# Performance work log

Hardware: AMD Instinct MI355X
Metric: run time of the kernel (lower is better)

The kernel has to match this reference:

```python
import jax, jax.numpy as jnp
import numpy as np

N = 30000      # num_nodes
E = 480000     # num_edges
NF = 128       # node_features
EF = 64        # edge_features
HID = 256      # hidden_dim
L = 4          # num_layers
H = 8          # heads
D = HID // H   # per-head dim = 32
SCALE = 0.02


def _ln(x, g, b, eps=1e-5):
    m = x.mean(-1, keepdims=True)
    v = ((x - m) ** 2).mean(-1, keepdims=True)
    return (x - m) * jax.lax.rsqrt(v + eps) * g + b


def _mlp_head(x, W1, b1, W2, b2):
    return jax.nn.sigmoid(jax.nn.relu(x @ W1 + b1) @ W2 + b2)


def setup_inputs() -> dict:
    key = jax.random.key(0)
    ks = jax.random.split(key, 32)
    r = lambda k, shp: SCALE * jax.random.normal(k, shp, dtype=jnp.float32)
    inp = {
        'x': jax.random.normal(ks[0], (N, NF), dtype=jnp.float32),
        'edge_attr': jax.random.normal(ks[1], (E, EF), dtype=jnp.float32),
        'edge_index': jax.random.randint(ks[2], (2, E), 0, N, dtype=jnp.int32),
        # encoders
        'enc_Wn': r(ks[3], (NF, HID)), 'enc_bn': jnp.zeros((HID,), jnp.float32),
        'enc_We': r(ks[4], (EF, HID)), 'enc_be': jnp.zeros((HID,), jnp.float32),
        # stacked TransformerConv params for L layers
        'Wq': r(ks[5], (L, HID, HID)), 'bq': jnp.zeros((L, HID), jnp.float32),
        'Wk': r(ks[6], (L, HID, HID)), 'bk': jnp.zeros((L, HID), jnp.float32),
        'Wv': r(ks[7], (L, HID, HID)), 'bv': jnp.zeros((L, HID), jnp.float32),
        'We': r(ks[8], (L, HID, HID)),  # lin_edge has no bias in PyG
        'Wsk': r(ks[9], (L, HID, HID)), 'bsk': jnp.zeros((L, HID), jnp.float32),
        # shared LayerNorm (module reuses self.norm every layer)
        'ln_g': jnp.ones((HID,), jnp.float32), 'ln_b': jnp.zeros((HID,), jnp.float32),
        # contagion predictor
        'cp_W1': r(ks[10], (HID, HID // 2)), 'cp_b1': jnp.zeros((HID // 2,), jnp.float32),
        'cp_W2': r(ks[11], (HID // 2, 1)), 'cp_b2': jnp.zeros((1,), jnp.float32),
        # systemic risk predictor
        'sp_W1': r(ks[12], (HID, HID // 2)), 'sp_b1': jnp.zeros((HID // 2,), jnp.float32),
        'sp_W2': r(ks[13], (HID // 2, 1)), 'sp_b2': jnp.zeros((1,), jnp.float32),
    }
    return inp


def reference(x, edge_attr, edge_index, enc_Wn, enc_bn, enc_We, enc_be,
              Wq, bq, Wk, bk, Wv, bv, We, Wsk, bsk, ln_g, ln_b,
              cp_W1, cp_b1, cp_W2, cp_b2, sp_W1, sp_b1, sp_W2, sp_b2):
    src, dst = edge_index[0], edge_index[1]
    h = x @ enc_Wn + enc_bn                 # [N,HID]
    e = edge_attr @ enc_We + enc_be         # [E,HID]
    inv_sqrt_d = 1.0 / jnp.sqrt(jnp.asarray(D, h.dtype))
    for l in range(L):
        # TransformerConv: query at dst, key/value at src, edge bias on both k and v
        q = (h @ Wq[l] + bq[l]).reshape(N, H, D)[dst]            # [E,H,D]
        ke = (e @ We[l]).reshape(E, H, D)                        # [E,H,D]
        k = (h @ Wk[l] + bk[l]).reshape(N, H, D)[src] + ke
        v = (h @ Wv[l] + bv[l]).reshape(N, H, D)[src] + ke
        score = (q * k).sum(-1) * inv_sqrt_d                     # [E,H]
        smax = jax.ops.segment_max(score, dst, num_segments=N)   # [N,H]
        p = jnp.exp(score - smax[dst])
        denom = jax.ops.segment_sum(p, dst, num_segments=N)
        alpha = p / (denom[dst] + 1e-16)                         # scatter-softmax
        agg = jax.ops.segment_sum(alpha[..., None] * v, dst, num_segments=N)
        out = agg.reshape(N, HID) + h @ Wsk[l] + bsk[l]          # concat heads + root skip
        h = _ln(h + out, ln_g, ln_b)                             # residual + shared LN (eval: no dropout)
    g = h.mean(0, keepdims=True)                                 # [1,HID] global mean pool
    contagion_risk = _mlp_head(h, cp_W1, cp_b1, cp_W2, cp_b2)    # [N,1]
    systemic_risk = _mlp_head(g, sp_W1, sp_b1, sp_W2, sp_b2)     # [1,1]
    return h, g, contagion_risk, systemic_risk
```

## Files before the change

kernel.cpp:

```cpp
#include <hip/hip_runtime.h>
#include <cstddef>
#include <cstdint>

#define NN 30000
#define EE 480000
#define NFD 128
#define EFD 64
#define HID 256
#define NL 4
#define NH 8

#define DT_BF16 0
#define DT_F32  1
#define DT_EXT  2

#define OFF_WT  ((size_t)65787648)
#define MIN_B   ((size_t)68015872)
#define MIN_A   ((size_t)129455872)

#define WT_ENC 0
#define WT_LAYER(l) (32768 + (size_t)(l) * 262144)
#define WT_CP1 (32768 + (size_t)1048576)

typedef short bf16x8 __attribute__((ext_vector_type(8)));
typedef unsigned short us8 __attribute__((ext_vector_type(8)));
typedef float f32x4 __attribute__((ext_vector_type(4)));

__device__ __forceinline__ float bf2f(unsigned short u) {
  union { unsigned int i; float f; } v; v.i = ((unsigned int)u) << 16; return v.f;
}
__device__ __forceinline__ unsigned short f2bf(float f) {
  union { float f; unsigned int i; } v; v.f = f;
  unsigned int i = v.i;
  return (unsigned short)((i + 0x7FFFu + ((i >> 16) & 1u)) >> 16);
}
struct F4 { float x, y, z, w; };
__device__ __forceinline__ F4 load4bf(const unsigned short* p) {
  ushort4 u = *reinterpret_cast<const ushort4*>(p);
  F4 f; f.x = bf2f(u.x); f.y = bf2f(u.y); f.z = bf2f(u.z); f.w = bf2f(u.w);
  return f;
}
__device__ __forceinline__ F4 load4f(const float* p) {
  float4 t = *reinterpret_cast<const float4*>(p);
  F4 f; f.x = t.x; f.y = t.y; f.z = t.z; f.w = t.w; return f;
}
__device__ __forceinline__ F4 load4any(const void* p, size_t idx, int f32) {
  return f32 ? load4f((const float*)p + idx) : load4bf((const unsigned short*)p + idx);
}
__device__ __forceinline__ float load1any(const void* p, size_t idx, int f32) {
  return f32 ? ((const float*)p)[idx] : bf2f(((const unsigned short*)p)[idx]);
}
__device__ __forceinline__ void store1any(void* p, size_t idx, float v, int f32) {
  if (f32) ((float*)p)[idx] = v; else ((unsigned short*)p)[idx] = f2bf(v);
}

__global__ void probe_dtype(const void* __restrict__ ln_g, int* __restrict__ flag) {
  unsigned int u = *(const unsigned int*)ln_g;
  *flag = ((u & 0xFFFFu) == 0u) ? 1 : 0;
}

__global__ void wt_build(const void* __restrict__ enc_Wn,
                         const void* __restrict__ Wq, const void* __restrict__ Wk,
                         const void* __restrict__ Wv, const void* __restrict__ Wsk,
                         const void* __restrict__ cp_W1,
                         unsigned short* __restrict__ Wt, const int* __restrict__ flagp)
{
  const int f = *flagp;
  size_t idx = (size_t)blockIdx.x * 256 + threadIdx.x;
  if (idx < 32768) {
    int n = idx >> 7, k = idx & 127;
    Wt[WT_ENC + idx] = f2bf(load1any(enc_Wn, (size_t)k * 256 + n, f));
  } else if (idx < 32768 + 1048576) {
    size_t off = idx - 32768;
    int l = off >> 18;
    int which = (off >> 16) & 3;
    size_t e = off & 65535;
    int n = e >> 8, k = e & 255;
    const void* W = (which == 0) ? Wq : (which == 1) ? Wk : (which == 2) ? Wv : Wsk;
    Wt[idx] = f2bf(load1any(W, (size_t)l * 65536 + (size_t)k * 256 + n, f));
  } else if (idx < 32768 + 1048576 + 32768) {
    size_t e = idx - 32768 - 1048576;
    int n = e >> 8, k = e & 255;
    Wt[idx] = f2bf(load1any(cp_W1, (size_t)k * 128 + n, f));
  }
}

template<bool OUT_F32, bool RELU>
__global__ __launch_bounds__(256) void mfma_gemm(
    const void* __restrict__ Av, int aMode,
    const unsigned short* __restrict__ Bt,
    const void* __restrict__ biasv, size_t biasEl, int biasMode,
    void* __restrict__ Cv, int ldC, int cOff,
    int M, int K, const int* __restrict__ flagp)
{
  const int f = *flagp;
  const int aF32 = (aMode == DT_EXT) ? f : aMode;
  const int biF32 = (biasMode == DT_EXT) ? f : biasMode;

  __shared__ unsigned short Al[128][40];
  __shared__ unsigned short Bl[64][40];
  const int bm = blockIdx.x * 128;
  const int bn = blockIdx.y * 64;
  const int tid = threadIdx.x;
  const int wv = tid >> 6, lane = tid & 63;
  const int l16 = lane & 15, quad = lane >> 4;

  f32x4 acc[2][4];
#pragma unroll
  for (int i = 0; i < 2; i++)
#pragma unroll
    for (int j = 0; j < 4; j++) acc[i][j] = (f32x4){0.f, 0.f, 0.f, 0.f};

  const int ar = tid >> 1;
  const int ah = (tid & 1) << 4;
  const int bnr = tid >> 2;
  const int bk8 = (tid & 3) << 3;

  for (int k0 = 0; k0 < K; k0 += 32) {
    us8 w0, w1;
    int gr = bm + ar;
    if (gr < M) {
      if (!aF32) {
        const unsigned short* ap = (const unsigned short*)Av + (size_t)gr * K + k0 + ah;
        w0 = *(const us8*)ap;
        w1 = *(const us8*)(ap + 8);
      } else {
        const float* ap = (const float*)Av + (size_t)gr * K + k0 + ah;
        float4 u0 = *(const float4*)ap;
        float4 u1 = *(const float4*)(ap + 4);
        float4 u2 = *(const float4*)(ap + 8);
        float4 u3 = *(const float4*)(ap + 12);
        w0[0] = f2bf(u0.x); w0[1] = f2bf(u0.y); w0[2] = f2bf(u0.z); w0[3] = f2bf(u0.w);
        w0[4] = f2bf(u1.x); w0[5] = f2bf(u1.y); w0[6] = f2bf(u1.z); w0[7] = f2bf(u1.w);
        w1[0] = f2bf(u2.x); w1[1] = f2bf(u2.y); w1[2] = f2bf(u2.z); w1[3] = f2bf(u2.w);
        w1[4] = f2bf(u3.x); w1[5] = f2bf(u3.y); w1[6] = f2bf(u3.z); w1[7] = f2bf(u3.w);
      }
    } else {
      w0 = (us8)0; w1 = (us8)0;
    }
    *(us8*)&Al[ar][ah] = w0;
    *(us8*)&Al[ar][ah + 8] = w1;
    *(us8*)&Bl[bnr][bk8] = *(const us8*)&Bt[(size_t)(bn + bnr) * K + k0 + bk8];
    __syncthreads();

    bf16x8 a0 = *(const bf16x8*)&Al[wv * 32 + l16][quad * 8];
    bf16x8 a1 = *(const bf16x8*)&Al[wv * 32 + 16 + l16][quad * 8];
#pragma unroll
    for (int tn = 0; tn < 4; tn++) {
      bf16x8 b = *(const bf16x8*)&Bl[tn * 16 + l16][quad * 8];
      acc[0][tn] = __builtin_amdgcn_mfma_f32_16x16x32_bf16(a0, b, acc[0][tn], 0, 0, 0);
      acc[1][tn] = __builtin_amdgcn_mfma_f32_16x16x32_bf16(a1, b, acc[1][tn], 0, 0, 0);
    }
    __syncthreads();
  }

#pragma unroll
  for (int tm = 0; tm < 2; tm++) {
#pragma unroll
    for (int tn = 0; tn < 4; tn++) {
      int col = bn + tn * 16 + l16;
      float bias = load1any(biasv, biasEl + col, biF32);
#pragma unroll
      for (int r = 0; r < 4; r++) {
        int row = bm + wv * 32 + tm * 16 + quad * 4 + r;
        if (row < M) {
          float v = acc[tm][tn][r] + bias;
          if (RELU) v = fmaxf(v, 0.f);
          size_t off = (size_t)row * ldC + cOff + col;
          if (OUT_F32) ((float*)Cv)[off] = v;
          else ((unsigned short*)Cv)[off] = f2bf(v);
        }
      }
    }
  }
}

__global__ __launch_bounds__(256) void mfma_gemm_qkvs(
    const unsigned short* __restrict__ A,
    const unsigned short* __restrict__ Bt,
    const void* __restrict__ bq, const void* __restrict__ bk,
    const void* __restrict__ bv, const void* __restrict__ bsk, size_t biasEl,
    unsigned short* __restrict__ Qb, unsigned short* __restrict__ KVb,
    unsigned short* __restrict__ Sb,
    int M, const int* __restrict__ flagp)
{
  const int f = *flagp;
  __shared__ unsigned short Al[128][40];
  __shared__ unsigned short Bl[64][40];
  const int bm = blockIdx.x * 128;
  const int bnG = blockIdx.y * 64;
  const int which = bnG >> 8;
  const int bn = bnG & 255;
  const int tid = threadIdx.x;
  const int wv = tid >> 6, lane = tid & 63;
  const int l16 = lane & 15, quad = lane >> 4;

  f32x4 acc[2][4];
#pragma unroll
  for (int i = 0; i < 2; i++)
#pragma unroll
    for (int j = 0; j < 4; j++) acc[i][j] = (f32x4){0.f, 0.f, 0.f, 0.f};

  const int ar = tid >> 1;
  const int ah = (tid & 1) << 4;
  const int bnr = tid >> 2;
  const int bk8 = (tid & 3) << 3;
  const unsigned short* Bbase = Bt + (size_t)which * 65536;

  for (int k0 = 0; k0 < HID; k0 += 32) {
    us8 w0, w1;
    int gr = bm + ar;
    if (gr < M) {
      const unsigned short* ap = A + (size_t)gr * HID + k0 + ah;
      w0 = *(const us8*)ap;
      w1 = *(const us8*)(ap + 8);
    } else {
      w0 = (us8)0; w1 = (us8)0;
    }
    *(us8*)&Al[ar][ah] = w0;
    *(us8*)&Al[ar][ah + 8] = w1;
    *(us8*)&Bl[bnr][bk8] = *(const us8*)&Bbase[(size_t)(bn + bnr) * HID + k0 + bk8];
    __syncthreads();

    bf16x8 a0 = *(const bf16x8*)&Al[wv * 32 + l16][quad * 8];
    bf16x8 a1 = *(const bf16x8*)&Al[wv * 32 + 16 + l16][quad * 8];
#pragma unroll
    for (int tn = 0; tn < 4; tn++) {
      bf16x8 b = *(const bf16x8*)&Bl[tn * 16 + l16][quad * 8];
      acc[0][tn] = __builtin_amdgcn_mfma_f32_16x16x32_bf16(a0, b, acc[0][tn], 0, 0, 0);
      acc[1][tn] = __builtin_amdgcn_mfma_f32_16x16x32_bf16(a1, b, acc[1][tn], 0, 0, 0);
    }
    __syncthreads();
  }

  const void* biasv = (which == 0) ? bq : (which == 1) ? bk : (which == 2) ? bv : bsk;
  unsigned short* out = (which == 0) ? Qb : (which == 3) ? Sb : KVb;
  const int ldC = (which == 1 || which == 2) ? 512 : 256;
  const int cOff = (which == 2) ? 256 : 0;

#pragma unroll
  for (int tm = 0; tm < 2; tm++) {
#pragma unroll
    for (int tn = 0; tn < 4; tn++) {
      int col = bn + tn * 16 + l16;
      float bias = load1any(biasv, biasEl + col, f);
#pragma unroll
      for (int r = 0; r < 4; r++) {
        int row = bm + wv * 32 + tm * 16 + quad * 4 + r;
        if (row < M)
          out[(size_t)row * ldC + cOff + col] = f2bf(acc[tm][tn][r] + bias);
      }
    }
  }
}

__global__ void fold_kernel(const void* __restrict__ enc_We,
                            const void* __restrict__ enc_be,
                            const void* __restrict__ We_all,
                            float* __restrict__ Mfold, const int* __restrict__ flagp)
{
  const int f = *flagp;
  int idx = blockIdx.x * blockDim.x + threadIdx.x;
  if (idx >= NL * 65 * HID) return;
  int l = idx / (65 * HID);
  int rc = idx - l * 65 * HID;
  int row = rc >> 8;
  int col = rc & 255;
  size_t Wbase = (size_t)l * HID * HID;
  float acc = 0.f;
  if (row < 64) {
    for (int k = 0; k < HID; k++)
      acc += load1any(enc_We, (size_t)row * HID + k, f) * load1any(We_all, Wbase + (size_t)k * HID + col, f);
  } else {
    for (int k = 0; k < HID; k++)
      acc += load1any(enc_be, k, f) * load1any(We_all, Wbase + (size_t)k * HID + col, f);
  }
  Mfold[idx] = acc;
}

__global__ void hist_kernel(const int* __restrict__ dst, int* __restrict__ rp) {
  int e = blockIdx.x * 256 + threadIdx.x;
  if (e < EE) atomicAdd(&rp[dst[e]], 1);
}

__global__ __launch_bounds__(1024) void scan_kernel(int* __restrict__ rp) {
  __shared__ int part[1024];
  int t = threadIdx.x;
  int base = t * 30;
  int loc[30];
  int sum = 0;
#pragma unroll
  for (int i = 0; i < 30; i++) {
    int idx = base + i;
    int v = (idx < NN) ? rp[idx] : 0;
    loc[i] = v; sum += v;
  }
  part[t] = sum;
  __syncthreads();
  for (int off = 1; off < 1024; off <<= 1) {
    int v = (t >= off) ? part[t - off] : 0;
    __syncthreads();
    part[t] += v;
    __syncthreads();
  }
  int run = (t == 0) ? 0 : part[t - 1];
#pragma unroll
  for (int i = 0; i < 30; i++) {
    int idx = base + i;
    if (idx < NN) { rp[idx] = run; run += loc[i]; }
    else if (idx == NN) { rp[NN] = run; }
  }
}

__global__ void scatter_kernel(const int* __restrict__ src, const int* __restrict__ dst,
                               const int* __restrict__ rp, int* __restrict__ cnt2,
                               int2* __restrict__ sed) {
  int e = blockIdx.x * 256 + threadIdx.x;
  if (e >= EE) return;
  int d = dst[e];
  int pos = rp[d] + atomicAdd(&cnt2[d], 1);
  int2 v; v.x = src[e]; v.y = e;
  sed[pos] = v;
}

__global__ void ea_build(const int2* __restrict__ sed, const void* __restrict__ edge_attr,
                         unsigned short* __restrict__ ea_srt, const int* __restrict__ flagp) {
  const int f = *flagp;
  int gid = blockIdx.x * 256 + threadIdx.x;
  int pos = gid >> 4;
  int sub = (gid & 15) * 4;
  int e = sed[pos].y;
  F4 v = load4any(edge_attr, (size_t)e * EFD + sub, f);
  ushort4 o; o.x = f2bf(v.x); o.y = f2bf(v.y); o.z = f2bf(v.z); o.w = f2bf(v.w);
  *reinterpret_cast<ushort4*>(ea_srt + (size_t)pos * EFD + sub) = o;
}

template<bool SORTED>
__global__ __launch_bounds__(256, 6) void edge_fused(
    const int* __restrict__ rp, const int2* __restrict__ sed,
    const unsigned short* __restrict__ Qb, const unsigned short* __restrict__ KV,
    const unsigned short* __restrict__ ea_srt,
    const void* __restrict__ edge_attr,
    const float* __restrict__ Mf,
    const unsigned short* __restrict__ Sb,
    unsigned short* __restrict__ hb,
    const void* __restrict__ ln_g, const void* __restrict__ ln_b,
    const int* __restrict__ flagp)
{
  __shared__ float wl[4][8][68];
  const int f = *flagp;
  const int wv = __builtin_amdgcn_readfirstlane(threadIdx.x >> 6);
  const int nw = blockIdx.x * 4 + wv;
  const int lane = threadIdx.x & 63;
  const int hd = lane >> 3;
  const int j = lane & 7;
  const int jb = j << 3;
  const int c4 = lane * 4;

  const size_t rowb = (size_t)nw * HID;
  F4 q4 = load4bf(Qb + rowb + c4);

  float t8[8] = {0.f, 0.f, 0.f, 0.f, 0.f, 0.f, 0.f, 0.f};
#pragma unroll
  for (int cc = 0; cc < 8; cc++) {
    F4 qc = load4bf(Qb + rowb + hd * 32 + cc * 4);
#pragma unroll
    for (int kk = 0; kk < 8; kk++) {
      const float4 m4 = *reinterpret_cast<const float4*>(
          Mf + (size_t)(jb + kk) * HID + hd * 32 + cc * 4);
      float a = t8[kk];
      a = fmaf(m4.x, qc.x, a);
      a = fmaf(m4.y, qc.y, a);
      a = fmaf(m4.z, qc.z, a);
      a = fmaf(m4.w, qc.w, a);
      t8[kk] = a;
    }
  }
  float s0;
  {
    F4 b4 = load4f(Mf + (size_t)64 * HID + c4);
    s0 = q4.x * b4.x + q4.y * b4.y + q4.z * b4.z + q4.w * b4.w;
    s0 += __shfl_xor(s0, 1);
    s0 += __shfl_xor(s0, 2);
    s0 += __shfl_xor(s0, 4);
  }

  float accv[4] = {0.f, 0.f, 0.f, 0.f};
  float wacc[8] = {0.f, 0.f, 0.f, 0.f, 0.f, 0.f, 0.f, 0.f};
  float den = 0.f;
  const int beg = rp[nw], end = rp[nw + 1];

  if (beg < end) {
    const float scl = 0.17677669529663687f;
    int tA = beg;
    int tB = (beg + 1 < end) ? beg + 1 : beg;
    int sA = sed[tA].x;
    int sB = sed[tB].x;
    const unsigned short* kvp;
    kvp = KV + (size_t)sA * 512;
    F4 kA = load4bf(kvp + c4);
    F4 vA = load4bf(kvp + 256 + c4);
    kvp = KV + (size_t)sB * 512;
    F4 kB = load4bf(kvp + c4);
    F4 vB = load4bf(kvp + 256 + c4);
    F4 ea0A, ea1A, ea0B, ea1B;
    if (SORTED) {
      ea0A = load4bf(ea_srt + (size_t)tA * EFD + j * 8);
      ea1A = load4bf(ea_srt + (size_t)tA * EFD + j * 8 + 4);
      ea0B = load4bf(ea_srt + (size_t)tB * EFD + j * 8);
      ea1B = load4bf(ea_srt + (size_t)tB * EFD + j * 8 + 4);
    } else {
      size_t eA = (size_t)sed[tA].y, eB = (size_t)sed[tB].y;
      ea0A = load4any(edge_attr, eA * EFD + j * 8, f);
      ea1A = load4any(edge_attr, eA * EFD + j * 8 + 4, f);
      ea0B = load4any(edge_attr, eB * EFD + j * 8, f);
      ea1B = load4any(edge_attr, eB * EFD + j * 8 + 4, f);
    }
    int tC = (beg + 2 < end) ? beg + 2 : beg;
    int tD = (beg + 3 < end) ? beg + 3 : beg;
    int sC = sed[tC].x;
    int sD = sed[tD].x;

    for (int t = beg; t < end; t += 2) {
      kvp = KV + (size_t)sC * 512;
      F4 kC = load4bf(kvp + c4);
      F4 vC = load4bf(kvp + 256 + c4);
      kvp = KV + (size_t)sD * 512;
      F4 kD = load4bf(kvp + c4);
      F4 vD = load4bf(kvp + 256 + c4);
      F4 ea0C, ea1C, ea0D, ea1D;
      if (SORTED) {
        ea0C = load4bf(ea_srt + (size_t)tC * EFD + j * 8);
        ea1C = load4bf(ea_srt + (size_t)tC * EFD + j * 8 + 4);
        ea0D = load4bf(ea_srt + (size_t)tD * EFD + j * 8);
        ea1D = load4bf(ea_srt + (size_t)tD * EFD + j * 8 + 4);
      } else {
        size_t eC = (size_t)sed[tC].y, eD = (size_t)sed[tD].y;
        ea0C = load4any(edge_attr, eC * EFD + j * 8, f);
        ea1C = load4any(edge_attr, eC * EFD + j * 8 + 4, f);
        ea0D = load4any(edge_attr, eD * EFD + j * 8, f);
        ea1D = load4any(edge_attr, eD * EFD + j * 8 + 4, f);
      }
      int tE = (t + 4 < end) ? t + 4 : beg;
      int tF = (t + 5 < end) ? t + 5 : beg;
      int sE = sed[tE].x;
      int sF = sed[tF].x;

      float mB = (t + 1 < end) ? 1.f : 0.f;
      float rA = q4.x * kA.x + q4.y * kA.y + q4.z * kA.z + q4.w * kA.w;
      float rB = q4.x * kB.x + q4.y * kB.y + q4.z * kB.z + q4.w * kB.w;
      rA = fmaf(ea0A.x, t8[0], rA); rB = fmaf(ea0B.x, t8[0], rB);
      rA = fmaf(ea0A.y, t8[1], rA); rB = fmaf(ea0B.y, t8[1], rB);
      rA = fmaf(ea0A.z, t8[2], rA); rB = fmaf(ea0B.z, t8[2], rB);
      rA = fmaf(ea0A.w, t8[3], rA); rB = fmaf(ea0B.w, t8[3], rB);
      rA = fmaf(ea1A.x, t8[4], rA); rB = fmaf(ea1B.x, t8[4], rB);
      rA = fmaf(ea1A.y, t8[5], rA); rB = fmaf(ea1B.y, t8[5], rB);
      rA = fmaf(ea1A.z, t8[6], rA); rB = fmaf(ea1B.z, t8[6], rB);
      rA = fmaf(ea1A.w, t8[7], rA); rB = fmaf(ea1B.w, t8[7], rB);
      { float u = __shfl_xor(rA, 1); float v = __shfl_xor(rB, 1); rA += u; rB += v; }
      { float u = __shfl_xor(rA, 2); float v = __shfl_xor(rB, 2); rA += u; rB += v; }
      { float u = __shfl_xor(rA, 4); float v = __shfl_xor(rB, 4); rA += u; rB += v; }
      float scA = fminf(fmaxf((rA + s0) * scl, -30.f), 30.f);
      float scB = fminf(fmaxf((rB + s0) * scl, -30.f), 30.f);
      float pA = __expf(scA);
      float pB = mB * __expf(scB);
      den += pA + pB;
      accv[0] = fmaf(pA, vA.x, fmaf(pB, vB.x, accv[0]));
      accv[1] = fmaf(pA, vA.y, fmaf(pB, vB.y, accv[1]));
      accv[2] = fmaf(pA, vA.z, fmaf(pB, vB.z, accv[2]));
      accv[3] = fmaf(pA, vA.w, fmaf(pB, vB.w, accv[3]));
      wacc[0] = fmaf(pA, ea0A.x, fmaf(pB, ea0B.x, wacc[0]));
      wacc[1] = fmaf(pA, ea0A.y, fmaf(pB, ea0B.y, wacc[1]));
      wacc[2] = fmaf(pA, ea0A.z, fmaf(pB, ea0B.z, wacc[2]));
      wacc[3] = fmaf(pA, ea0A.w, fmaf(pB, ea0B.w, wacc[3]));
      wacc[4] = fmaf(pA, ea1A.x, fmaf(pB, ea1B.x, wacc[4]));
      wacc[5] = fmaf(pA, ea1A.y, fmaf(pB, ea1B.y, wacc[5]));
      wacc[6] = fmaf(pA, ea1A.z, fmaf(pB, ea1B.z, wacc[6]));
      wacc[7] = fmaf(pA, ea1A.w, fmaf(pB, ea1B.w, wacc[7]));
      kA = kC; vA = vC; ea0A = ea0C; ea1A = ea1C;
      kB = kD; vB = vD; ea0B = ea0D; ea1B = ea1D;
      tA = tC; tB = tD; tC = tE; tD = tF; sC = sE; sD = sF;
    }
  }

#pragma unroll
  for (int i = 0; i < 8; i++) wl[wv][hd][jb + i] = wacc[i];
  __syncthreads();

  float ke0 = 0.f, ke1 = 0.f, ke2 = 0.f, ke3 = 0.f;
#pragma unroll 8
  for (int k = 0; k < 64; k++) {
    float w = wl[wv][hd][k];
    float4 m4 = *reinterpret_cast<const float4*>(Mf + (size_t)k * HID + c4);
    ke0 = fmaf(w, m4.x, ke0);
    ke1 = fmaf(w, m4.y, ke1);
    ke2 = fmaf(w, m4.z, ke2);
    ke3 = fmaf(w, m4.w, ke3);
  }

  float invden = 1.f / (den + 1e-16f);
  float sel = (end > beg) ? 1.f : 0.f;
  F4 b4 = load4f(Mf + (size_t)64 * HID + c4);
  F4 s4 = load4bf(Sb + rowb + c4);
  F4 hh = load4bf(hb + rowb + c4);
  float r0 = hh.x + sel * ((accv[0] + ke0) * invden + b4.x) + s4.x;
  float r1 = hh.y + sel * ((accv[1] + ke1) * invden + b4.y) + s4.y;
  float r2 = hh.z + sel * ((accv[2] + ke2) * invden + b4.z) + s4.z;
  float r3 = hh.w + sel * ((accv[3] + ke3) * invden + b4.w) + s4.w;

  float sum = r0 + r1 + r2 + r3;
#pragma unroll
  for (int o = 1; o < 64; o <<= 1) sum += __shfl_xor(sum, o);
  float mean = sum * (1.f / HID);
  float d0 = r0 - mean, d1 = r1 - mean, d2 = r2 - mean, d3 = r3 - mean;
  float vs = d0 * d0 + d1 * d1 + d2 * d2 + d3 * d3;
#pragma unroll
  for (int o = 1; o < 64; o <<= 1) vs += __shfl_xor(vs, o);
  float rstd = rsqrtf(vs * (1.f / HID) + 1e-5f);
  ushort4 o4;
  o4.x = f2bf(d0 * rstd * load1any(ln_g, c4 + 0, f) + load1any(ln_b, c4 + 0, f));
  o4.y = f2bf(d1 * rstd * load1any(ln_g, c4 + 1, f) + load1any(ln_b, c4 + 1, f));
  o4.z = f2bf(d2 * rstd * load1any(ln_g, c4 + 2, f) + load1any(ln_b, c4 + 2, f));
  o4.w = f2bf(d3 * rstd * load1any(ln_g, c4 + 3, f) + load1any(ln_b, c4 + 3, f));
  *reinterpret_cast<ushort4*>(hb + rowb + c4) = o4;
}

__global__ void copy_h_out(const unsigned short* __restrict__ h, void* __restrict__ out,
                           const int* __restrict__ flagp) {
  const int f = *flagp;
  int i = blockIdx.x * 256 + threadIdx.x;
  store1any(out, i, bf2f(h[i]), f);
}

__global__ void colsum_kernel(const unsigned short* __restrict__ h, float* __restrict__ gsum) {
  int c = threadIdx.x;
  float s = 0.f;
  for (int r = blockIdx.x; r < NN; r += gridDim.x) s += bf2f(h[(size_t)r * HID + c]);
  atomicAdd(&gsum[c], s);
}

__global__ void write_g_kernel(const float* __restrict__ gsum, void* __restrict__ out,
                               const int* __restrict__ flagp) {
  const int f = *flagp;
  int c = threadIdx.x;
  store1any(out, (size_t)NN * HID + c, gsum[c] * (1.f / NN), f);
}

__global__ __launch_bounds__(256) void cp2_kernel(
    const float* __restrict__ hid, const void* __restrict__ W2,
    const void* __restrict__ b2, void* __restrict__ out,
    const int* __restrict__ flagp)
{
  const int f = *flagp;
  int nw = (blockIdx.x << 2) + (threadIdx.x >> 6);
  if (nw >= NN) return;
  int lane = threadIdx.x & 63;
  const float* hr = hid + (size_t)nw * 128;
  float s = hr[lane * 2] * load1any(W2, lane * 2, f) + hr[lane * 2 + 1] * load1any(W2, lane * 2 + 1, f);
#pragma unroll
  for (int o = 1; o < 64; o <<= 1) s += __shfl_xor(s, o);
  if (lane == 0) {
    float xv = s + load1any(b2, 0, f);
    store1any(out, (size_t)NN * HID + HID + nw, 1.f / (1.f + __expf(-xv)), f);
  }
}

__global__ __launch_bounds__(128) void sys_kernel(
    const float* __restrict__ gsum,
    const void* __restrict__ W1, const void* __restrict__ b1,
    const void* __restrict__ W2, const void* __restrict__ b2,
    void* __restrict__ out, const int* __restrict__ flagp)
{
  const int f = *flagp;
  __shared__ float red[2];
  int j = threadIdx.x;
  float acc = load1any(b1, j, f);
  const float invN = 1.f / NN;
  for (int k = 0; k < HID; k++) acc = fmaf(gsum[k] * invN, load1any(W1, (size_t)k * 128 + j, f), acc);
  float v = fmaxf(acc, 0.f) * load1any(W2, j, f);
#pragma unroll
  for (int o = 1; o < 64; o <<= 1) v += __shfl_xor(v, o);
  if ((j & 63) == 0) red[j >> 6] = v;
  __syncthreads();
  if (j == 0) {
    float xv = red[0] + red[1] + load1any(b2, 0, f);
    store1any(out, (size_t)NN * HID + HID + NN, 1.f / (1.f + __expf(-xv)), f);
  }
}

__global__ void diag_kernel(float* __restrict__ out, float v, int n4) {
  int i = blockIdx.x * 256 + threadIdx.x;
  if (i < n4) out[i] = (i == 0) ? v : 0.f;
}

extern "C" void kernel_launch(void* const* d_in, const int* in_sizes, int n_in,
                              void* d_out, int out_size, void* d_ws, size_t ws_size,
                              hipStream_t stream)
{
  (void)in_sizes; (void)n_in;

  if (ws_size < MIN_B) {
    diag_kernel<<<(out_size / 2 + 255) / 256, 256, 0, stream>>>(
        (float*)d_out, (float)(ws_size >> 20), out_size / 2);
    return;
  }
  const bool planA = (ws_size >= MIN_A);

  const void* x         = d_in[0];
  const void* edge_attr = d_in[1];
  const int*  edge_index= (const int*)d_in[2];
  const void* enc_Wn = d_in[3];
  const void* enc_bn = d_in[4];
  const void* enc_We = d_in[5];
  const void* enc_be = d_in[6];
  const void* Wq  = d_in[7];
  const void* bq  = d_in[8];
  const void* Wk  = d_in[9];
  const void* bk  = d_in[10];
  const void* Wv  = d_in[11];
  const void* bvv = d_in[12];
  const void* We  = d_in[13];
  const void* Wsk = d_in[14];
  const void* bsk = d_in[15];
  const void* ln_g = d_in[16];
  const void* ln_b = d_in[17];
  const void* cp_W1 = d_in[18];
  const void* cp_b1 = d_in[19];
  const void* cp_W2 = d_in[20];
  const void* cp_b2 = d_in[21];
  const void* sp_W1 = d_in[22];
  const void* sp_b1 = d_in[23];
  const void* sp_W2 = d_in[24];
  const void* sp_b2 = d_in[25];

  char* ws = (char*)d_ws;
  unsigned short* hb  = (unsigned short*)(ws + 0);
  unsigned short* Sb  = (unsigned short*)(ws + 15360000);
  unsigned short* KVb = (unsigned short*)(ws + 30720000);
  int2*  sed   = (int2*)(ws + 61440000);
  int*   rp    = (int*)(ws + 65280000);
  int*   cnt2  = (int*)(ws + 65400064);
  float* Mfold = (float*)(ws + 65520128);
  float* gsum  = (float*)(ws + 65786368);
  int*   flagp = (int*)(ws + 65787392);
  unsigned short* Wt = (unsigned short*)(ws + OFF_WT);
  unsigned short* ea_srt = (unsigned short*)(ws + MIN_B);
  unsigned short* Qb = (unsigned short*)d_out;
  float* cph = (float*)(ws + 15360000);

  const int* src = edge_index;
  const int* dst = edge_index + EE;

  probe_dtype<<<1, 1, 0, stream>>>(ln_g, flagp);
  wt_build<<<(1114112 + 255) / 256, 256, 0, stream>>>(enc_Wn, Wq, Wk, Wv, Wsk, cp_W1, Wt, flagp);
  fold_kernel<<<(NL * 65 * HID + 255) / 256, 256, 0, stream>>>(enc_We, enc_be, We, Mfold, flagp);

  hipMemsetAsync(rp, 0, 120064, stream);
  hipMemsetAsync(cnt2, 0, 120064, stream);
  hist_kernel<<<(EE + 255) / 256, 256, 0, stream>>>(dst, rp);
  scan_kernel<<<1, 1024, 0, stream>>>(rp);
  scatter_kernel<<<(EE + 255) / 256, 256, 0, stream>>>(src, dst, rp, cnt2, sed);
  if (planA) {
    ea_build<<<EE * 16 / 256, 256, 0, stream>>>(sed, edge_attr, ea_srt, flagp);
  }

  const int gx = (NN + 127) / 128;
  {
    dim3 g(gx, 4);
    mfma_gemm<false, false><<<g, 256, 0, stream>>>(
        x, DT_EXT, Wt + WT_ENC, enc_bn, 0, DT_EXT, hb, HID, 0, NN, NFD, flagp);
  }

  for (int l = 0; l < NL; l++) {
    size_t bo = (size_t)l * HID;
    dim3 gQ(gx, 16);
    mfma_gemm_qkvs<<<gQ, 256, 0, stream>>>(
        hb, Wt + WT_LAYER(l), bq, bk, bvv, bsk, bo, Qb, KVb, Sb, NN, flagp);
    const float* Mf = Mfold + (size_t)l * 65 * HID;
    if (planA) {
      edge_fused<true><<<NN / 4, 256, 0, stream>>>(
          rp, sed, Qb, KVb, ea_srt, edge_attr, Mf, Sb, hb, ln_g, ln_b, flagp);
    } else {
      edge_fused<false><<<NN / 4, 256, 0, stream>>>(
          rp, sed, Qb, KVb, ea_srt, edge_attr, Mf, Sb, hb, ln_g, ln_b, flagp);
    }
  }

  copy_h_out<<<NN, 256, 0, stream>>>(hb, d_out, flagp);
  hipMemsetAsync(gsum, 0, HID * 4, stream);
  colsum_kernel<<<256, 256, 0, stream>>>(hb, gsum);
  write_g_kernel<<<1, 256, 0, stream>>>(gsum, d_out, flagp);

  {
    dim3 g(gx, 2);
    mfma_gemm<true, true><<<g, 256, 0, stream>>>(
        hb, DT_BF16, Wt + WT_CP1, cp_b1, 0, DT_EXT, cph, 128, 0, NN, HID, flagp);
  }
  cp2_kernel<<<NN / 4, 256, 0, stream>>>(cph, cp_W2, cp_b2, d_out, flagp);
  sys_kernel<<<1, 128, 0, stream>>>(gsum, sp_W1, sp_b1, sp_W2, sp_b2, d_out, flagp);
}
```

Before: 2.474 ms.

## Sort destination nodes by in-degree so waves in a block get similar work

Adds a counting sort of nodes by in-degree (histogram, descending scan, scatter into a permutation) and makes edge_fused look up its node through this permutation, so the four waves of a block handle nodes of similar degree. This targets load imbalance, where a block is held by its longest wave at the __syncthreads. It also restructures the q·M fold loop to load the per-head q slice into registers once, hoists the bias load, and drops the occupancy hint from launch bounds. In exchange it adds several small launches, reuses the cnt2 buffer for perm and the output buffer for the histogram, and may raise register pressure.

Measured after the change: 2.286 ms. -7.6%, faster.

```diff
diff --git a/kernel.cpp b/kernel.cpp
--- a/kernel.cpp
+++ b/kernel.cpp
@@ -323,6 +323,33 @@
   sed[pos] = v;
 }
 
+__global__ void deg_hist(const int* __restrict__ rp, int* __restrict__ dh) {
+  int n = blockIdx.x * 256 + threadIdx.x;
+  if (n < NN) {
+    int d = rp[n + 1] - rp[n]; if (d > 255) d = 255;
+    atomicAdd(&dh[d], 1);
+  }
+}
+__global__ __launch_bounds__(256) void deg_scan(const int* __restrict__ dh,
+                                                int* __restrict__ dcnt) {
+  __shared__ int h[256];
+  int t = threadIdx.x;
+  h[t] = dh[t];
+  __syncthreads();
+  int s = 0;
+  for (int d = t + 1; d < 256; d++) s += h[d];
+  dcnt[t] = s;
+}
+__global__ void deg_scatter(const int* __restrict__ rp, int* __restrict__ dcnt,
+                            int* __restrict__ perm) {
+  int n = blockIdx.x * 256 + threadIdx.x;
+  if (n < NN) {
+    int d = rp[n + 1] - rp[n]; if (d > 255) d = 255;
+    int pos = atomicAdd(&dcnt[d], 1);
+    perm[pos] = n;
+  }
+}
+
 __global__ void ea_build(const int2* __restrict__ sed, const void* __restrict__ edge_attr,
                          unsigned short* __restrict__ ea_srt, const int* __restrict__ flagp) {
   const int f = *flagp;
@@ -336,8 +363,9 @@
 }
 
 template<bool SORTED>
-__global__ __launch_bounds__(256, 6) void edge_fused(
+__global__ __launch_bounds__(256) void edge_fused(
     const int* __restrict__ rp, const int2* __restrict__ sed,
+    const int* __restrict__ perm,
     const unsigned short* __restrict__ Qb, const unsigned short* __restrict__ KV,
     const unsigned short* __restrict__ ea_srt,
     const void* __restrict__ edge_attr,
@@ -349,41 +377,42 @@
 {
   __shared__ float wl[4][8][68];
   const int f = *flagp;
-  const int wv = __builtin_amdgcn_readfirstlane(threadIdx.x >> 6);
-  const int nw = blockIdx.x * 4 + wv;
+  const int wv = threadIdx.x >> 6;
+  const int nw = perm[blockIdx.x * 4 + wv];
   const int lane = threadIdx.x & 63;
   const int hd = lane >> 3;
   const int j = lane & 7;
-  const int jb = j << 3;
   const int c4 = lane * 4;
 
   const size_t rowb = (size_t)nw * HID;
   F4 q4 = load4bf(Qb + rowb + c4);
 
-  float t8[8] = {0.f, 0.f, 0.f, 0.f, 0.f, 0.f, 0.f, 0.f};
-#pragma unroll
-  for (int cc = 0; cc < 8; cc++) {
-    F4 qc = load4bf(Qb + rowb + hd * 32 + cc * 4);
-#pragma unroll
-    for (int kk = 0; kk < 8; kk++) {
-      const float4 m4 = *reinterpret_cast<const float4*>(
-          Mf + (size_t)(jb + kk) * HID + hd * 32 + cc * 4);
-      float a = t8[kk];
-      a = fmaf(m4.x, qc.x, a);
-      a = fmaf(m4.y, qc.y, a);
-      a = fmaf(m4.z, qc.z, a);
-      a = fmaf(m4.w, qc.w, a);
-      t8[kk] = a;
-    }
-  }
-  float s0;
-  {
-    F4 b4 = load4f(Mf + (size_t)64 * HID + c4);
-    s0 = q4.x * b4.x + q4.y * b4.y + q4.z * b4.z + q4.w * b4.w;
-    s0 += __shfl_xor(s0, 1);
-    s0 += __shfl_xor(s0, 2);
-    s0 += __shfl_xor(s0, 4);
-  }
+  float q32[32];
+#pragma unroll
+  for (int i = 0; i < 8; i++) {
+    F4 t = load4bf(Qb + rowb + hd * 32 + i * 4);
+    q32[i * 4 + 0] = t.x; q32[i * 4 + 1] = t.y; q32[i * 4 + 2] = t.z; q32[i * 4 + 3] = t.w;
+  }
+  float t8[8];
+#pragma unroll
+  for (int kk = 0; kk < 8; kk++) {
+    const float* Mrow = Mf + (size_t)(j * 8 + kk) * HID + hd * 32;
+    float a = 0.f;
+#pragma unroll
+    for (int cc = 0; cc < 8; cc++) {
+      float4 m4 = *reinterpret_cast<const float4*>(Mrow + cc * 4);
+      a = fmaf(m4.x, q32[cc * 4 + 0], a);
+      a = fmaf(m4.y, q32[cc * 4 + 1], a);
+      a = fmaf(m4.z, q32[cc * 4 + 2], a);
+      a = fmaf(m4.w, q32[cc * 4 + 3], a);
+    }
+    t8[kk] = a;
+  }
+  F4 b4 = load4f(Mf + (size_t)64 * HID + c4);
+  float s0 = q4.x * b4.x + q4.y * b4.y + q4.z * b4.z + q4.w * b4.w;
+  s0 += __shfl_xor(s0, 1);
+  s0 += __shfl_xor(s0, 2);
+  s0 += __shfl_xor(s0, 4);
 
   float accv[4] = {0.f, 0.f, 0.f, 0.f};
   float wacc[8] = {0.f, 0.f, 0.f, 0.f, 0.f, 0.f, 0.f, 0.f};
@@ -484,7 +513,7 @@
   }
 
 #pragma unroll
-  for (int i = 0; i < 8; i++) wl[wv][hd][jb + i] = wacc[i];
+  for (int i = 0; i < 8; i++) wl[wv][hd][j * 8 + i] = wacc[i];
   __syncthreads();
 
   float ke0 = 0.f, ke1 = 0.f, ke2 = 0.f, ke3 = 0.f;
@@ -500,7 +529,6 @@
 
   float invden = 1.f / (den + 1e-16f);
   float sel = (end > beg) ? 1.f : 0.f;
-  F4 b4 = load4f(Mf + (size_t)64 * HID + c4);
   F4 s4 = load4bf(Sb + rowb + c4);
   F4 hh = load4bf(hb + rowb + c4);
   float r0 = hh.x + sel * ((accv[0] + ke0) * invden + b4.x) + s4.x;
@@ -646,6 +674,9 @@
   unsigned short* Wt = (unsigned short*)(ws + OFF_WT);
   unsigned short* ea_srt = (unsigned short*)(ws + MIN_B);
   unsigned short* Qb = (unsigned short*)d_out;
+  int* dhist = (int*)((char*)d_out + 15360000);
+  int* dcnt  = dhist + 256;
+  int* perm  = cnt2;
   float* cph = (float*)(ws + 15360000);
 
   const int* src = edge_index;
@@ -660,6 +691,12 @@
   hist_kernel<<<(EE + 255) / 256, 256, 0, stream>>>(dst, rp);
   scan_kernel<<<1, 1024, 0, stream>>>(rp);
   scatter_kernel<<<(EE + 255) / 256, 256, 0, stream>>>(src, dst, rp, cnt2, sed);
+
+  hipMemsetAsync(dhist, 0, 1024, stream);
+  deg_hist<<<(NN + 255) / 256, 256, 0, stream>>>(rp, dhist);
+  deg_scan<<<1, 256, 0, stream>>>(dhist, dcnt);
+  deg_scatter<<<(NN + 255) / 256, 256, 0, stream>>>(rp, dcnt, perm);
+
   if (planA) {
     ea_build<<<EE * 16 / 256, 256, 0, stream>>>(sed, edge_attr, ea_srt, flagp);
   }
@@ -679,10 +716,10 @@
     const float* Mf = Mfold + (size_t)l * 65 * HID;
     if (planA) {
       edge_fused<true><<<NN / 4, 256, 0, stream>>>(
-          rp, sed, Qb, KVb, ea_srt, edge_attr, Mf, Sb, hb, ln_g, ln_b, flagp);
+          rp, sed, perm, Qb, KVb, ea_srt, edge_attr, Mf, Sb, hb, ln_g, ln_b, flagp);
     } else {
       edge_fused<false><<<NN / 4, 256, 0, stream>>>(
-          rp, sed, Qb, KVb, ea_srt, edge_attr, Mf, Sb, hb, ln_g, ln_b, flagp);
+          rp, sed, perm, Qb, KVb, ea_srt, edge_attr, Mf, Sb, hb, ln_g, ln_b, flagp);
     }
   }
 
```
